# Optimization experiments

Hardware: AMD Instinct MI355X
Metric: run time of the kernel (lower is better)

## Reference

```python
import jax, jax.numpy as jnp
import numpy as np

# Static multi-scale pyramid (H, W) per level
SPATIAL_SHAPES = [(100, 100), (50, 50), (25, 25), (13, 13), (7, 7)]
D, H, L, P = 256, 8, 5, 4   # d_model, heads, levels, points
HD = D // H
B = 4
LQ = sum(h * w for h, w in SPATIAL_SHAPES)  # 13343
DFF = 2048


def layer_norm(x, g, b, eps=1e-5):
    m = x.mean(-1, keepdims=True)
    v = ((x - m) ** 2).mean(-1, keepdims=True)
    return (x - m) / jnp.sqrt(v + eps) * g + b


def ms_deform_attn_core(value, loc, attn):
    """value: [B, Lin, H, HD]; loc: [B, LQ, H, L, P, 2] in [0,1]; attn: [B, LQ, H, L, P].
    Bilinear sampling matches F.grid_sample(align_corners=False, padding_mode='zeros')."""
    out = jnp.zeros((B, H, LQ, HD), dtype=value.dtype)
    start = 0
    for lvl, (H_, W_) in enumerate(SPATIAL_SHAPES):
        val = value[:, start:start + H_ * W_]            # [B, HW, H, HD]
        start += H_ * W_
        val = val.transpose(0, 2, 1, 3)                   # [B, H, HW, HD]
        l = loc[:, :, :, lvl]                             # [B, LQ, H, P, 2]
        px = l[..., 0] * W_ - 0.5                         # grid_sample unnormalize
        py = l[..., 1] * H_ - 0.5
        x0 = jnp.floor(px)
        y0 = jnp.floor(py)
        wx1 = px - x0
        wy1 = py - y0
        x0i = x0.astype(jnp.int32)
        y0i = y0.astype(jnp.int32)
        samples = jnp.zeros((B, H, LQ, P, HD), dtype=value.dtype)
        for dy in (0, 1):
            for dx in (0, 1):
                xi = x0i + dx
                yi = y0i + dy
                w = (wx1 if dx else 1.0 - wx1) * (wy1 if dy else 1.0 - wy1)
                valid = (xi >= 0) & (xi < W_) & (yi >= 0) & (yi < H_)
                idx = jnp.clip(yi, 0, H_ - 1) * W_ + jnp.clip(xi, 0, W_ - 1)  # [B, LQ, H, P]
                idx_t = idx.transpose(0, 2, 1, 3).reshape(B, H, LQ * P)
                g = jnp.take_along_axis(val, idx_t[..., None], axis=2)        # [B, H, LQ*P, HD]
                g = g.reshape(B, H, LQ, P, HD)
                w_t = jnp.where(valid, w, 0.0).transpose(0, 2, 1, 3)          # [B, H, LQ, P]
                samples = samples + g * w_t[..., None]
        aw = attn[:, :, :, lvl].transpose(0, 2, 1, 3)     # [B, H, LQ, P]
        out = out + jnp.sum(samples * aw[..., None], axis=3)
    return out.transpose(0, 2, 1, 3).reshape(B, LQ, H * HD)


def setup_inputs() -> dict:
    key = jax.random.key(0)
    ks = jax.random.split(key, 24)
    s = 0.02
    inp = {
        'src': jax.random.normal(ks[0], (B, LQ, D), jnp.float32),
        'pos': jax.random.normal(ks[1], (B, LQ, D), jnp.float32),
        'reference_points': jax.random.uniform(ks[2], (B, LQ, L, 2), jnp.float32),
        'spatial_shapes': jnp.array(SPATIAL_SHAPES, dtype=jnp.int32),
        'level_start_index': jnp.array(np.cumsum([0] + [h * w for h, w in SPATIAL_SHAPES[:-1]]), dtype=jnp.int32),
        'W_off': jax.random.normal(ks[3], (D, H * L * P * 2), jnp.float32) * s,
        'b_off': jax.random.normal(ks[4], (H * L * P * 2,), jnp.float32) * s,
        'W_attn': jax.random.normal(ks[5], (D, H * L * P), jnp.float32) * s,
        'b_attn': jax.random.normal(ks[6], (H * L * P,), jnp.float32) * s,
        'W_val': jax.random.normal(ks[7], (D, D), jnp.float32) * s,
        'b_val': jax.random.normal(ks[8], (D,), jnp.float32) * s,
        'W_out': jax.random.normal(ks[9], (D, D), jnp.float32) * s,
        'b_out': jax.random.normal(ks[10], (D,), jnp.float32) * s,
        'g1': jnp.ones((D,), jnp.float32),
        'beta1': jnp.zeros((D,), jnp.float32),
        'W1': jax.random.normal(ks[11], (D, DFF), jnp.float32) * s,
        'bl1': jax.random.normal(ks[12], (DFF,), jnp.float32) * s,
        'W2': jax.random.normal(ks[13], (DFF, D), jnp.float32) * s,
        'bl2': jax.random.normal(ks[14], (D,), jnp.float32) * s,
        'g2': jnp.ones((D,), jnp.float32),
        'beta2': jnp.zeros((D,), jnp.float32),
    }
    return inp


def reference(src, pos, reference_points, spatial_shapes, level_start_index,
              W_off, b_off, W_attn, b_attn, W_val, b_val, W_out, b_out,
              g1, beta1, W1, bl1, W2, bl2, g2, beta2):
    q = src + pos                                                    # with_pos_embed
    off = (q @ W_off + b_off).reshape(B, LQ, H, L, P, 2)
    attn = jax.nn.softmax((q @ W_attn + b_attn).reshape(B, LQ, H, L * P), axis=-1)
    attn = attn.reshape(B, LQ, H, L, P)
    value = (src @ W_val + b_val).reshape(B, LQ, H, HD)
    # offset normalizer is (W, H) per level
    norm = jnp.array([[w, h] for h, w in SPATIAL_SHAPES], dtype=src.dtype)  # [L, 2]
    loc = reference_points[:, :, None, :, None, :] + off / norm[None, None, None, :, None, :]
    attn_out = ms_deform_attn_core(value, loc, attn) @ W_out + b_out
    x = layer_norm(src + attn_out, g1, beta1)                        # dropout = identity (eval)
    ffn = jax.nn.relu(x @ W1 + bl1) @ W2 + bl2
    return layer_norm(x + ffn, g2, beta2)
```

## Files before the change

### kernel.cpp

```cpp
#include <hip/hip_runtime.h>
#include <hip/hip_bf16.h>

typedef __bf16 bf16_t;
typedef __bf16 bf16x8 __attribute__((ext_vector_type(8)));
typedef float f32x4 __attribute__((ext_vector_type(4)));

#define B_    4
#define LQ_   13343
#define D_    256
#define H_    8
#define HD_   32
#define DFF_  2048
#define M_    (B_ * LQ_)

__device__ __forceinline__ int xcd_swz(int orig, int nwg) {
  int q = nwg >> 3, r = nwg & 7;
  int xcd = orig & 7, idx = orig >> 3;
  return (xcd < r ? xcd * (q + 1) : r * (q + 1) + (xcd - r) * q) + idx;
}

#define BM 128
#define BN 128
#define BK 32

#define MODE_F32       0
#define MODE_BF16      2
#define MODE_BF16_RELU 3

__device__ __forceinline__ void gload_lds16(const void* g, void* l) {
  __builtin_amdgcn_global_load_lds(
      (const __attribute__((address_space(1))) void*)g,
      (__attribute__((address_space(3))) void*)l, 16, 0, 0);
}

template <int MODE, bool AF32>
__global__ __launch_bounds__(256) void gemm_bt(
    const void* __restrict__ Av, int lda,
    const bf16_t* __restrict__ Bt, int ldb,
    const float* __restrict__ bias,
    void* __restrict__ Cv, int ldc,
    int M, int N, int K)
{
  __shared__ alignas(16) bf16_t As[2][BM * BK];
  __shared__ alignas(16) bf16_t Bs[2][BN * BK];
  const int tid  = threadIdx.x;
  const int wave = tid >> 6, lane = tid & 63;
  const int nyb = (N + BN - 1) / BN;
  const int gid = xcd_swz(blockIdx.x, (int)gridDim.x);
  const int m0 = (gid / nyb) * BM;
  const int n0 = (gid - (gid / nyb) * nyb) * BN;
  const int wm = (wave & 1) * 64;
  const int wn = (wave >> 1) * 64;
  const int lrow = lane & 15;
  const int quad = lane >> 4;

  const int srow = wave * 16 + (lane >> 2);
  const int scol = (lane & 3) * 8;
  const bf16_t* Ab = (const bf16_t*)Av;
  const float*  Af = (const float*)Av;

  const int ar0 = min(m0 + srow,      M - 1);
  const int ar1 = min(m0 + srow + 64, M - 1);
  const int br0 = min(n0 + srow,      N - 1);
  const int br1 = min(n0 + srow + 64, N - 1);

  const int r0 = tid >> 2;
  const int kc = (tid & 3) * 8;
  const int arw0 = min(m0 + r0,      M - 1);
  const int arw1 = min(m0 + r0 + 64, M - 1);

  auto stage_async = [&](int ke, int buf) {
    if (!AF32) {
      gload_lds16(Ab + (size_t)ar0 * lda + ke + scol, &As[buf][wave * 512]);
      gload_lds16(Ab + (size_t)ar1 * lda + ke + scol, &As[buf][2048 + wave * 512]);
    }
    gload_lds16(Bt + (size_t)br0 * ldb + ke + scol, &Bs[buf][wave * 512]);
    gload_lds16(Bt + (size_t)br1 * ldb + ke + scol, &Bs[buf][2048 + wave * 512]);
  };

  if (AF32) {
    const f32x4* p0 = (const f32x4*)(Af + (size_t)arw0 * lda + kc);
    const f32x4* p1 = (const f32x4*)(Af + (size_t)arw1 * lda + kc);
    f32x4 u0 = p0[0], w0 = p0[1], u1 = p1[0], w1 = p1[1];
    bf16x8 a0, a1;
#pragma unroll
    for (int j = 0; j < 4; ++j) {
      a0[j] = (bf16_t)u0[j]; a0[j + 4] = (bf16_t)w0[j];
      a1[j] = (bf16_t)u1[j]; a1[j + 4] = (bf16_t)w1[j];
    }
    *(bf16x8*)(&As[0][r0 * BK + kc])        = a0;
    *(bf16x8*)(&As[0][(r0 + 64) * BK + kc]) = a1;
  }
  stage_async(0, 0);
  __syncthreads();

  f32x4 acc[4][4] = {};
  const int nkt = K / BK;
  for (int kt = 0; kt < nkt; ++kt) {
    const int cur = kt & 1, nxt = cur ^ 1;
    const bool more = (kt + 1) < nkt;
    f32x4 u0 = {}, w0 = {}, u1 = {}, w1 = {};
    if (more) {
      const int ke = (kt + 1) * BK;
      if (AF32) {
        const f32x4* p0 = (const f32x4*)(Af + (size_t)arw0 * lda + ke + kc);
        const f32x4* p1 = (const f32x4*)(Af + (size_t)arw1 * lda + ke + kc);
        u0 = p0[0]; w0 = p0[1]; u1 = p1[0]; w1 = p1[1];
      }
      stage_async(ke, nxt);
    }
    bf16x8 af[4], bfr[4];
#pragma unroll
    for (int i = 0; i < 4; ++i)
      af[i] = *(const bf16x8*)(&As[cur][(wm + i * 16 + lrow) * BK + quad * 8]);
#pragma unroll
    for (int j = 0; j < 4; ++j)
      bfr[j] = *(const bf16x8*)(&Bs[cur][(wn + j * 16 + lrow) * BK + quad * 8]);
#pragma unroll
    for (int i = 0; i < 4; ++i)
#pragma unroll
      for (int j = 0; j < 4; ++j)
        acc[i][j] = __builtin_amdgcn_mfma_f32_16x16x32_bf16(af[i], bfr[j], acc[i][j], 0, 0, 0);
    if (more && AF32) {
      bf16x8 a0, a1;
#pragma unroll
      for (int j = 0; j < 4; ++j) {
        a0[j] = (bf16_t)u0[j]; a0[j + 4] = (bf16_t)w0[j];
        a1[j] = (bf16_t)u1[j]; a1[j + 4] = (bf16_t)w1[j];
      }
      *(bf16x8*)(&As[nxt][r0 * BK + kc])        = a0;
      *(bf16x8*)(&As[nxt][(r0 + 64) * BK + kc]) = a1;
    }
    __syncthreads();
  }

  float*  Cf = (float*)Cv;
  bf16_t* Cb = (bf16_t*)Cv;
#pragma unroll
  for (int i = 0; i < 4; ++i) {
#pragma unroll
    for (int j = 0; j < 4; ++j) {
      int gn = n0 + wn + j * 16 + lrow;
      if (gn >= N) continue;
      float bv = bias ? bias[gn] : 0.f;
#pragma unroll
      for (int r = 0; r < 4; ++r) {
        int gm = m0 + wm + i * 16 + quad * 4 + r;
        if (gm >= M) continue;
        float v = acc[i][j][r] + bv;
        size_t ci = (size_t)gm * ldc + gn;
        if (MODE == MODE_F32)       Cf[ci] = v;
        else if (MODE == MODE_BF16) Cb[ci] = (bf16_t)v;
        else                        Cb[ci] = (bf16_t)(v > 0.f ? v : 0.f);
      }
    }
  }
}

__global__ __launch_bounds__(256) void gemm_qkv(
    const float* __restrict__ src, const float* __restrict__ pos,
    const bf16_t* __restrict__ Bt,
    const float* __restrict__ b_off, const float* __restrict__ b_attn,
    bf16_t* __restrict__ offb, float* __restrict__ attnb)
{
  __shared__ alignas(16) bf16_t As[2][BM * BK];
  __shared__ alignas(16) bf16_t Bs[2][BN * BK];
  const int tid  = threadIdx.x;
  const int wave = tid >> 6, lane = tid & 63;
  const int gid = xcd_swz(blockIdx.x, (int)gridDim.x);
  const int m0 = (gid >> 2) * BM;
  const int n0 = (gid & 3) * BN;
  const int wm = (wave & 1) * 64;
  const int wn = (wave >> 1) * 64;
  const int lrow = lane & 15;
  const int quad = lane >> 4;
  const int N = 480;

  const int srow = wave * 16 + (lane >> 2);
  const int scol = (lane & 3) * 8;
  const int br0 = min(n0 + srow,      N - 1);
  const int br1 = min(n0 + srow + 64, N - 1);
  const int r0 = tid >> 2;
  const int kc = (tid & 3) * 8;
  const int arw0 = min(m0 + r0,      M_ - 1);
  const int arw1 = min(m0 + r0 + 64, M_ - 1);

  auto stageB = [&](int ke, int buf) {
    gload_lds16(Bt + (size_t)br0 * 256 + ke + scol, &Bs[buf][wave * 512]);
    gload_lds16(Bt + (size_t)br1 * 256 + ke + scol, &Bs[buf][2048 + wave * 512]);
  };
  auto loadA = [&](int ke, f32x4& u0, f32x4& w0, f32x4& u1, f32x4& w1) {
    const f32x4* s0 = (const f32x4*)(src + (size_t)arw0 * 256 + ke + kc);
    const f32x4* p0 = (const f32x4*)(pos + (size_t)arw0 * 256 + ke + kc);
    const f32x4* s1 = (const f32x4*)(src + (size_t)arw1 * 256 + ke + kc);
    const f32x4* p1 = (const f32x4*)(pos + (size_t)arw1 * 256 + ke + kc);
    u0 = s0[0] + p0[0]; w0 = s0[1] + p0[1];
    u1 = s1[0] + p1[0]; w1 = s1[1] + p1[1];
  };
  auto writeA = [&](int buf, f32x4 u0, f32x4 w0, f32x4 u1, f32x4 w1) {
    bf16x8 a0, a1;
#pragma unroll
    for (int j = 0; j < 4; ++j) {
      a0[j] = (bf16_t)u0[j]; a0[j + 4] = (bf16_t)w0[j];
      a1[j] = (bf16_t)u1[j]; a1[j + 4] = (bf16_t)w1[j];
    }
    *(bf16x8*)(&As[buf][r0 * BK + kc])        = a0;
    *(bf16x8*)(&As[buf][(r0 + 64) * BK + kc]) = a1;
  };

  { f32x4 u0, w0, u1, w1; loadA(0, u0, w0, u1, w1); writeA(0, u0, w0, u1, w1); }
  stageB(0, 0);
  __syncthreads();

  f32x4 acc[4][4] = {};
  for (int kt = 0; kt < 8; ++kt) {
    const int cur = kt & 1, nxt = cur ^ 1;
    const bool more = kt < 7;
    f32x4 u0 = {}, w0 = {}, u1 = {}, w1 = {};
    if (more) { loadA((kt + 1) * BK, u0, w0, u1, w1); stageB((kt + 1) * BK, nxt); }
    bf16x8 af[4], bfr[4];
#pragma unroll
    for (int i = 0; i < 4; ++i)
      af[i] = *(const bf16x8*)(&As[cur][(wm + i * 16 + lrow) * BK + quad * 8]);
#pragma unroll
    for (int j = 0; j < 4; ++j)
      bfr[j] = *(const bf16x8*)(&Bs[cur][(wn + j * 16 + lrow) * BK + quad * 8]);
#pragma unroll
    for (int i = 0; i < 4; ++i)
#pragma unroll
      for (int j = 0; j < 4; ++j)
        acc[i][j] = __builtin_amdgcn_mfma_f32_16x16x32_bf16(af[i], bfr[j], acc[i][j], 0, 0, 0);
    if (more) writeA(nxt, u0, w0, u1, w1);
    __syncthreads();
  }

#pragma unroll
  for (int i = 0; i < 4; ++i) {
#pragma unroll
    for (int j = 0; j < 4; ++j) {
      int gn = n0 + wn + j * 16 + lrow;
      if (gn >= N) continue;
      float bv = (gn < 320) ? b_off[gn] : b_attn[gn - 320];
#pragma unroll
      for (int r = 0; r < 4; ++r) {
        int gm = m0 + wm + i * 16 + quad * 4 + r;
        if (gm >= M_) continue;
        float v = acc[i][j][r] + bv;
        if (gn < 320) offb[(size_t)gm * 320 + gn] = (bf16_t)v;
        else          attnb[(size_t)gm * 160 + gn - 320] = v;
      }
    }
  }
}

__global__ __launch_bounds__(256) void k_ffn(
    const bf16_t* __restrict__ x,
    const bf16_t* __restrict__ w1t,
    const float* __restrict__ bl1,
    const bf16_t* __restrict__ w2t,
    float* __restrict__ outf)
{
  __shared__ alignas(16) bf16_t xs[8][64 * 32];
  __shared__ alignas(16) bf16_t hs[4][64 * 32];
  __shared__ alignas(16) bf16_t wst[2][256 * 32];
  const int tid  = threadIdx.x;
  const int wave = tid >> 6, lane = tid & 63;
  const int lrow = lane & 15, quad = lane >> 4;
  const int m0 = xcd_swz(blockIdx.x, (int)gridDim.x) * 64;
  const int srow = lane >> 2;
  const int scol = (lane & 3) * 8;
  const int wc0 = wave * 64;

  auto stage_w1 = [&](int hc, int kt, int buf) {
#pragma unroll
    for (int c = 0; c < 2; ++c) {
      int r = c * 64 + wave * 16 + srow;
      gload_lds16(w1t + (size_t)(hc * 128 + r) * 256 + kt * 32 + scol,
                  &wst[buf][c * 2048 + wave * 512]);
    }
  };
  auto stage_w2 = [&](int hc, int kt2, int buf) {
#pragma unroll
    for (int c = 0; c < 4; ++c) {
      int r = c * 64 + wave * 16 + srow;
      gload_lds16(w2t + (size_t)r * 2048 + hc * 128 + kt2 * 32 + scol,
                  &wst[buf][c * 2048 + wave * 512]);
    }
  };

  {
    int gr = min(m0 + wave * 16 + srow, M_ - 1);
#pragma unroll
    for (int c = 0; c < 8; ++c)
      gload_lds16(x + (size_t)gr * 256 + c * 32 + scol, &xs[c][wave * 512]);
  }
  stage_w1(0, 0, 0);
  __syncthreads();

  f32x4 cacc[4][4] = {};
  int s = 0;
  for (int hc = 0; hc < 16; ++hc) {
    float b0 = bl1[hc * 128 + wave * 32 + lrow];
    float b1 = bl1[hc * 128 + wave * 32 + 16 + lrow];
    f32x4 hacc[4][2] = {};
    for (int kt = 0; kt < 8; ++kt) {
      const int cur = s & 1, nxt = cur ^ 1;
      if (kt < 7) stage_w1(hc, kt + 1, nxt);
      else        stage_w2(hc, 0, nxt);
      bf16x8 af[4], bf[2];
#pragma unroll
      for (int i = 0; i < 4; ++i)
        af[i] = *(const bf16x8*)(&xs[kt][(i * 16 + lrow) * 32 + quad * 8]);
#pragma unroll
      for (int j = 0; j < 2; ++j)
        bf[j] = *(const bf16x8*)(&wst[cur][(wave * 32 + j * 16 + lrow) * 32 + quad * 8]);
#pragma unroll
      for (int i = 0; i < 4; ++i)
#pragma unroll
        for (int j = 0; j < 2; ++j)
          hacc[i][j] = __builtin_amdgcn_mfma_f32_16x16x32_bf16(af[i], bf[j], hacc[i][j], 0, 0, 0);
      if (kt == 7) {
#pragma unroll
        for (int i = 0; i < 4; ++i)
#pragma unroll
          for (int j = 0; j < 2; ++j) {
            float bb = j ? b1 : b0;
#pragma unroll
            for (int r = 0; r < 4; ++r) {
              float v = hacc[i][j][r] + bb;
              hs[wave][(i * 16 + quad * 4 + r) * 32 + j * 16 + lrow] =
                  (bf16_t)(v > 0.f ? v : 0.f);
            }
          }
      }
      __syncthreads();
      ++s;
    }
    for (int kt2 = 0; kt2 < 4; ++kt2) {
      const int cur = s & 1, nxt = cur ^ 1;
      if (kt2 < 3)      stage_w2(hc, kt2 + 1, nxt);
      else if (hc < 15) stage_w1(hc + 1, 0, nxt);
      bf16x8 af2[4], bf2[4];
#pragma unroll
      for (int i = 0; i < 4; ++i)
        af2[i] = *(const bf16x8*)(&hs[kt2][(i * 16 + lrow) * 32 + quad * 8]);
#pragma unroll
      for (int j = 0; j < 4; ++j)
        bf2[j] = *(const bf16x8*)(&wst[cur][(wc0 + j * 16 + lrow) * 32 + quad * 8]);
#pragma unroll
      for (int i = 0; i < 4; ++i)
#pragma unroll
        for (int j = 0; j < 4; ++j)
          cacc[i][j] = __builtin_amdgcn_mfma_f32_16x16x32_bf16(af2[i], bf2[j], cacc[i][j], 0, 0, 0);
      __syncthreads();
      ++s;
    }
  }

#pragma unroll
  for (int i = 0; i < 4; ++i)
#pragma unroll
    for (int j = 0; j < 4; ++j)
#pragma unroll
      for (int r = 0; r < 4; ++r) {
        int gm = m0 + i * 16 + quad * 4 + r;
        if (gm < M_) outf[(size_t)gm * 256 + wc0 + j * 16 + lrow] = cacc[i][j][r];
      }
}

__global__ __launch_bounds__(256) void k_transpose_all(
    const float* __restrict__ i0, const float* __restrict__ i1,
    const float* __restrict__ i2, const float* __restrict__ i3,
    const float* __restrict__ i4, const float* __restrict__ i5,
    bf16_t* __restrict__ o0, bf16_t* __restrict__ o1, bf16_t* __restrict__ o2,
    bf16_t* __restrict__ o3, bf16_t* __restrict__ o4, bf16_t* __restrict__ o5)
{
  int bid = blockIdx.x;
  const float* in; bf16_t* out; int K, N, txn;
  if (bid < 80)        { in = i0; out = o0; K = 256;  N = 320;  txn = 10; }
  else if (bid < 120)  { in = i1; out = o1; K = 256;  N = 160;  bid -= 80;  txn = 5; }
  else if (bid < 184)  { in = i2; out = o2; K = 256;  N = 256;  bid -= 120; txn = 8; }
  else if (bid < 248)  { in = i3; out = o3; K = 256;  N = 256;  bid -= 184; txn = 8; }
  else if (bid < 760)  { in = i4; out = o4; K = 256;  N = 2048; bid -= 248; txn = 64; }
  else                 { in = i5; out = o5; K = 2048; N = 256;  bid -= 760; txn = 8; }
  const int bx = bid % txn, by = bid / txn;
  __shared__ float tile[32][33];
  const int k0 = by * 32, n0 = bx * 32;
  const int tx = threadIdx.x & 31, ty = threadIdx.x >> 5;
#pragma unroll
  for (int r = ty; r < 32; r += 8)
    tile[r][tx] = in[(size_t)(k0 + r) * N + n0 + tx];
  __syncthreads();
#pragma unroll
  for (int r = ty; r < 32; r += 8)
    out[(size_t)(n0 + r) * K + k0 + tx] = (bf16_t)tile[tx][r];
}

__global__ __launch_bounds__(256) void k_sample(
    const bf16_t* __restrict__ value,
    const bf16_t* __restrict__ off,
    const float* __restrict__ attn,
    const float* __restrict__ rp,
    bf16_t* __restrict__ core)
{
  const int Wl[5] = {100, 50, 25, 13, 7};
  const int st[5] = {0, 10000, 12500, 13125, 13294};
  __shared__ alignas(16) bf16_t s_off[8][320];
  __shared__ alignas(16) float  s_attn[8][160];
  __shared__ float s_rp[8][10];
  const int t = threadIdx.x;
  const int bq0 = xcd_swz(blockIdx.x, (int)gridDim.x) * 8;
  for (int i = t; i < 320; i += 256) {
    int q = i / 40, e = i - q * 40;
    if (bq0 + q < M_) {
      *(bf16x8*)&s_off[q][e * 8] = *(const bf16x8*)(off + (size_t)(bq0 + q) * 320 + e * 8);
      *(f32x4*)&s_attn[q][e * 4] = *(const f32x4*)(attn + (size_t)(bq0 + q) * 160 + e * 4);
    }
  }
  if (t < 80) {
    int q = t / 10, e = t - q * 10;
    if (bq0 + q < M_) s_rp[q][e] = rp[(size_t)(bq0 + q) * 10 + e];
  }
  __syncthreads();
  if (t < 64) {
    float* p = &s_attn[t >> 3][(t & 7) * 20];
    float mx = p[0];
#pragma unroll
    for (int i = 1; i < 20; ++i) mx = fmaxf(mx, p[i]);
    float e[20], sum = 0.f;
#pragma unroll
    for (int i = 0; i < 20; ++i) { e[i] = expf(p[i] - mx); sum += e[i]; }
    float inv = 1.f / sum;
#pragma unroll
    for (int i = 0; i < 20; ++i) p[i] = e[i] * inv;
  }
  __syncthreads();

  const int wq = t >> 5, s = t & 31;
  const int h = s >> 2, d0 = (s & 3) * 8;
  const int bq = bq0 + wq;
  if (bq >= M_) return;
  const int b = bq / LQ_;
  const bf16_t* vbase = value + ((size_t)b * LQ_) * 256 + h * 32 + d0;
  float acc[8] = {};
#pragma unroll
  for (int lvl = 0; lvl < 5; ++lvl) {
    const float W = (float)Wl[lvl];
    const float rx = s_rp[wq][lvl * 2], ry = s_rp[wq][lvl * 2 + 1];
#pragma unroll
    for (int p = 0; p < 4; ++p) {
      const int base = (h * 5 + lvl) * 4 + p;
      float px = rx * W + (float)s_off[wq][base * 2]     - 0.5f;
      float py = ry * W + (float)s_off[wq][base * 2 + 1] - 0.5f;
      float aw = s_attn[wq][h * 20 + lvl * 4 + p];
      float x0f = floorf(px), y0f = floorf(py);
      float wx1 = px - x0f, wy1 = py - y0f;
      int x0 = (int)x0f, y0 = (int)y0f;
#pragma unroll
      for (int dy = 0; dy < 2; ++dy) {
        int yi = y0 + dy;
        bool vy = (yi >= 0) & (yi < Wl[lvl]);
        int yc = min(max(yi, 0), Wl[lvl] - 1);
        float wy = dy ? wy1 : 1.f - wy1;
#pragma unroll
        for (int dx = 0; dx < 2; ++dx) {
          int xi = x0 + dx;
          bool vx = (xi >= 0) & (xi < Wl[lvl]);
          int xc = min(max(xi, 0), Wl[lvl] - 1);
          float cw = (vx & vy) ? aw * wy * (dx ? wx1 : 1.f - wx1) : 0.f;
          bf16x8 v = *(const bf16x8*)(vbase + (size_t)(st[lvl] + yc * Wl[lvl] + xc) * 256);
#pragma unroll
          for (int j = 0; j < 8; ++j) acc[j] += cw * (float)v[j];
        }
      }
    }
  }
  bf16x8 o;
#pragma unroll
  for (int j = 0; j < 8; ++j) o[j] = (bf16_t)acc[j];
  *(bf16x8*)(core + (size_t)bq * 256 + h * 32 + d0) = o;
}

template <typename TA, typename TR, typename TO>
__global__ __launch_bounds__(256) void k_ln4(
    const TA* __restrict__ a, const TR* __restrict__ res,
    const float* __restrict__ eb, const float* __restrict__ g,
    const float* __restrict__ beta, TO* __restrict__ out, int rows)
{
  const int wave = threadIdx.x >> 6, lane = threadIdx.x & 63;
  const int row = blockIdx.x * 4 + wave;
  if (row >= rows) return;
  const size_t base = (size_t)row * 256 + lane * 4;
  float v[4];
#pragma unroll
  for (int j = 0; j < 4; ++j) {
    v[j] = (float)a[base + j] + (float)res[base + j];
    if (eb) v[j] += eb[lane * 4 + j];
  }
  float s1 = v[0] + v[1] + v[2] + v[3];
  float s2 = v[0] * v[0] + v[1] * v[1] + v[2] * v[2] + v[3] * v[3];
#pragma unroll
  for (int o = 32; o > 0; o >>= 1) { s1 += __shfl_xor(s1, o); s2 += __shfl_xor(s2, o); }
  float m = s1 * (1.f / 256.f);
  float var = s2 * (1.f / 256.f) - m * m;
  float inv = rsqrtf(var + 1e-5f);
#pragma unroll
  for (int j = 0; j < 4; ++j)
    out[base + j] = (TO)(((v[j] - m) * inv) * g[lane * 4 + j] + beta[lane * 4 + j]);
}

extern "C" void kernel_launch(void* const* d_in, const int* in_sizes, int n_in,
                              void* d_out, int out_size, void* d_ws, size_t ws_size,
                              hipStream_t stream) {
  const float* src   = (const float*)d_in[0];
  const float* pos   = (const float*)d_in[1];
  const float* rp    = (const float*)d_in[2];
  const float* W_off = (const float*)d_in[5];
  const float* b_off = (const float*)d_in[6];
  const float* W_attn= (const float*)d_in[7];
  const float* b_attn= (const float*)d_in[8];
  const float* W_val = (const float*)d_in[9];
  const float* b_val = (const float*)d_in[10];
  const float* W_out = (const float*)d_in[11];
  const float* b_out = (const float*)d_in[12];
  const float* g1    = (const float*)d_in[13];
  const float* beta1 = (const float*)d_in[14];
  const float* W1    = (const float*)d_in[15];
  const float* bl1   = (const float*)d_in[16];
  const float* W2    = (const float*)d_in[17];
  const float* bl2   = (const float*)d_in[18];
  const float* g2    = (const float*)d_in[19];
  const float* beta2 = (const float*)d_in[20];

  char* ws = (char*)d_ws;
  const size_t SZ_TOK = (size_t)M_ * 256 * 2;
  const size_t SZ_ATT = (size_t)M_ * 160 * 4;

  size_t o = 0;
  bf16_t* wTqkv = (bf16_t*)(ws + o); o += 480 * 256 * 2;
  bf16_t* wTval = (bf16_t*)(ws + o); o += 256 * 256 * 2;
  bf16_t* wTout = (bf16_t*)(ws + o); o += 256 * 256 * 2;
  bf16_t* wT1   = (bf16_t*)(ws + o); o += 2048 * 256 * 2;
  bf16_t* wT2   = (bf16_t*)(ws + o); o += 2048 * 256 * 2;
  o = (o + 255) & ~(size_t)255;
  char* Areg = ws + o; o += SZ_TOK;
  char* Creg = ws + o; o += SZ_ATT;
  char* Dreg = ws + o; o += SZ_TOK;

  bf16_t* coreb   = (bf16_t*)Areg;
  float*  attnb   = (float*) Creg;
  bf16_t* attn_out= (bf16_t*)Creg;
  bf16_t* valb    = (bf16_t*)Dreg;
  bf16_t* xbuf    = (bf16_t*)Dreg;
  bf16_t* offb    = (bf16_t*)d_out;
  float*  outf    = (float*) d_out;

  k_transpose_all<<<dim3(1272), 256, 0, stream>>>(
      W_off, W_attn, W_val, W_out, W1, W2,
      wTqkv, wTqkv + 320 * 256, wTval, wTout, wT1, wT2);

  dim3 blk(256);
  const int gM = (M_ + BM - 1) / BM;

  gemm_qkv<<<dim3(gM * 4), blk, 0, stream>>>(src, pos, wTqkv, b_off, b_attn, offb, attnb);
  gemm_bt<MODE_BF16, true><<<dim3(gM * 2), blk, 0, stream>>>(src, 256, wTval, 256, b_val, valb, 256, M_, 256, 256);
  k_sample<<<dim3((M_ + 7) / 8), blk, 0, stream>>>(valb, offb, attnb, rp, coreb);
  gemm_bt<MODE_BF16, false><<<dim3(gM * 2), blk, 0, stream>>>(coreb, 256, wTout, 256, b_out, attn_out, 256, M_, 256, 256);
  k_ln4<float, bf16_t, bf16_t><<<dim3((M_ + 3) / 4), blk, 0, stream>>>(src, attn_out, (const float*)nullptr, g1, beta1, xbuf, M_);

  k_ffn<<<dim3((M_ + 63) / 64), blk, 0, stream>>>(xbuf, wT1, bl1, wT2, outf);

  k_ln4<bf16_t, float, float><<<dim3((M_ + 3) / 4), blk, 0, stream>>>(xbuf, outf, bl2, g2, beta2, outf, M_);
}
```

Baseline: 711.4 us.

## Load FFN weights directly from global to registers and swizzle LDS tiles

Removes the double-buffered LDS weight staging in the fused FFN kernel. Each wave now reads its W1/W2 fragments straight from global memory (relying on L2 since all blocks share the weights), and the per-k-step barriers are dropped. The x and hidden tiles in LDS use an XOR swizzle to avoid bank conflicts, and the launch bounds ask for 3 blocks per CU now that LDS use is smaller. The risk is higher global and L2 load latency on the MFMA critical path with no prefetching, and possible register pressure from the occupancy hint.

Result: slower. 786.2 us (+10.5%).

```diff
diff --git a/kernel.cpp b/kernel.cpp
--- a/kernel.cpp
+++ b/kernel.cpp
@@ -253,7 +253,8 @@
   }
 }
 
-__global__ __launch_bounds__(256) void k_ffn(
+#define SWZ(row, byte) ((byte) ^ (((row) & 7) << 4))
+__global__ __launch_bounds__(256, 3) void k_ffn(
     const bf16_t* __restrict__ x,
     const bf16_t* __restrict__ w1t,
     const float* __restrict__ bl1,
@@ -262,7 +263,6 @@
 {
   __shared__ alignas(16) bf16_t xs[8][64 * 32];
   __shared__ alignas(16) bf16_t hs[4][64 * 32];
-  __shared__ alignas(16) bf16_t wst[2][256 * 32];
   const int tid  = threadIdx.x;
   const int wave = tid >> 6, lane = tid & 63;
   const int lrow = lane & 15, quad = lane >> 4;
@@ -271,89 +271,82 @@
   const int scol = (lane & 3) * 8;
   const int wc0 = wave * 64;
 
-  auto stage_w1 = [&](int hc, int kt, int buf) {
-#pragma unroll
-    for (int c = 0; c < 2; ++c) {
-      int r = c * 64 + wave * 16 + srow;
-      gload_lds16(w1t + (size_t)(hc * 128 + r) * 256 + kt * 32 + scol,
-                  &wst[buf][c * 2048 + wave * 512]);
-    }
-  };
-  auto stage_w2 = [&](int hc, int kt2, int buf) {
-#pragma unroll
-    for (int c = 0; c < 4; ++c) {
-      int r = c * 64 + wave * 16 + srow;
-      gload_lds16(w2t + (size_t)r * 2048 + hc * 128 + kt2 * 32 + scol,
-                  &wst[buf][c * 2048 + wave * 512]);
-    }
-  };
-
   {
-    int gr = min(m0 + wave * 16 + srow, M_ - 1);
-#pragma unroll
-    for (int c = 0; c < 8; ++c)
-      gload_lds16(x + (size_t)gr * 256 + c * 32 + scol, &xs[c][wave * 512]);
-  }
-  stage_w1(0, 0, 0);
+    const int row = wave * 16 + srow;
+    const int gr = min(m0 + row, M_ - 1);
+    const int wb = SWZ(row, row * 64 + scol * 2);
+#pragma unroll
+    for (int c = 0; c < 8; ++c) {
+      bf16x8 v = *(const bf16x8*)(x + (size_t)gr * 256 + c * 32 + scol);
+      *(bf16x8*)((char*)&xs[c][0] + wb) = v;
+    }
+  }
+
+  const bf16_t* w1r0 = w1t + (size_t)(wave * 32 + lrow) * 256 + quad * 8;
+  const bf16_t* w1r1 = w1t + (size_t)(wave * 32 + 16 + lrow) * 256 + quad * 8;
+  const bf16_t* w2r0 = w2t + (size_t)(wc0 + lrow) * 2048 + quad * 8;
+  const bf16_t* w2r1 = w2r0 + (size_t)16 * 2048;
+  const bf16_t* w2r2 = w2r0 + (size_t)32 * 2048;
+  const bf16_t* w2r3 = w2r0 + (size_t)48 * 2048;
+
   __syncthreads();
 
   f32x4 cacc[4][4] = {};
-  int s = 0;
   for (int hc = 0; hc < 16; ++hc) {
-    float b0 = bl1[hc * 128 + wave * 32 + lrow];
-    float b1 = bl1[hc * 128 + wave * 32 + 16 + lrow];
+    const float b0 = bl1[hc * 128 + wave * 32 + lrow];
+    const float b1 = bl1[hc * 128 + wave * 32 + 16 + lrow];
+    const size_t w1off = (size_t)hc * 128 * 256;
     f32x4 hacc[4][2] = {};
+#pragma unroll
     for (int kt = 0; kt < 8; ++kt) {
-      const int cur = s & 1, nxt = cur ^ 1;
-      if (kt < 7) stage_w1(hc, kt + 1, nxt);
-      else        stage_w2(hc, 0, nxt);
-      bf16x8 af[4], bf[2];
-#pragma unroll
-      for (int i = 0; i < 4; ++i)
-        af[i] = *(const bf16x8*)(&xs[kt][(i * 16 + lrow) * 32 + quad * 8]);
-#pragma unroll
-      for (int j = 0; j < 2; ++j)
-        bf[j] = *(const bf16x8*)(&wst[cur][(wave * 32 + j * 16 + lrow) * 32 + quad * 8]);
-#pragma unroll
-      for (int i = 0; i < 4; ++i)
-#pragma unroll
-        for (int j = 0; j < 2; ++j)
-          hacc[i][j] = __builtin_amdgcn_mfma_f32_16x16x32_bf16(af[i], bf[j], hacc[i][j], 0, 0, 0);
-      if (kt == 7) {
-#pragma unroll
-        for (int i = 0; i < 4; ++i)
-#pragma unroll
-          for (int j = 0; j < 2; ++j) {
-            float bb = j ? b1 : b0;
-#pragma unroll
-            for (int r = 0; r < 4; ++r) {
-              float v = hacc[i][j][r] + bb;
-              hs[wave][(i * 16 + quad * 4 + r) * 32 + j * 16 + lrow] =
-                  (bf16_t)(v > 0.f ? v : 0.f);
-            }
-          }
-      }
-      __syncthreads();
-      ++s;
-    }
+      bf16x8 bf0 = *(const bf16x8*)(w1r0 + w1off + kt * 32);
+      bf16x8 bf1 = *(const bf16x8*)(w1r1 + w1off + kt * 32);
+      bf16x8 af[4];
+#pragma unroll
+      for (int i = 0; i < 4; ++i) {
+        const int row = i * 16 + lrow;
+        af[i] = *(const bf16x8*)((char*)&xs[kt][0] + SWZ(row, row * 64 + quad * 16));
+      }
+#pragma unroll
+      for (int i = 0; i < 4; ++i) {
+        hacc[i][0] = __builtin_amdgcn_mfma_f32_16x16x32_bf16(af[i], bf0, hacc[i][0], 0, 0, 0);
+        hacc[i][1] = __builtin_amdgcn_mfma_f32_16x16x32_bf16(af[i], bf1, hacc[i][1], 0, 0, 0);
+      }
+    }
+    __syncthreads();
+#pragma unroll
+    for (int i = 0; i < 4; ++i)
+#pragma unroll
+      for (int j = 0; j < 2; ++j) {
+        const float bb = j ? b1 : b0;
+#pragma unroll
+        for (int r = 0; r < 4; ++r) {
+          float v = hacc[i][j][r] + bb;
+          const int row = i * 16 + quad * 4 + r;
+          *(bf16_t*)((char*)&hs[wave][0] + SWZ(row, row * 64 + (j * 16 + lrow) * 2)) =
+              (bf16_t)(v > 0.f ? v : 0.f);
+        }
+      }
+    __syncthreads();
+    const size_t w2off = (size_t)hc * 128;
+#pragma unroll
     for (int kt2 = 0; kt2 < 4; ++kt2) {
-      const int cur = s & 1, nxt = cur ^ 1;
-      if (kt2 < 3)      stage_w2(hc, kt2 + 1, nxt);
-      else if (hc < 15) stage_w1(hc + 1, 0, nxt);
-      bf16x8 af2[4], bf2[4];
-#pragma unroll
-      for (int i = 0; i < 4; ++i)
-        af2[i] = *(const bf16x8*)(&hs[kt2][(i * 16 + lrow) * 32 + quad * 8]);
-#pragma unroll
-      for (int j = 0; j < 4; ++j)
-        bf2[j] = *(const bf16x8*)(&wst[cur][(wc0 + j * 16 + lrow) * 32 + quad * 8]);
+      bf16x8 bf2[4];
+      bf2[0] = *(const bf16x8*)(w2r0 + w2off + kt2 * 32);
+      bf2[1] = *(const bf16x8*)(w2r1 + w2off + kt2 * 32);
+      bf2[2] = *(const bf16x8*)(w2r2 + w2off + kt2 * 32);
+      bf2[3] = *(const bf16x8*)(w2r3 + w2off + kt2 * 32);
+      bf16x8 af2[4];
+#pragma unroll
+      for (int i = 0; i < 4; ++i) {
+        const int row = i * 16 + lrow;
+        af2[i] = *(const bf16x8*)((char*)&hs[kt2][0] + SWZ(row, row * 64 + quad * 16));
+      }
 #pragma unroll
       for (int i = 0; i < 4; ++i)
 #pragma unroll
         for (int j = 0; j < 4; ++j)
           cacc[i][j] = __builtin_amdgcn_mfma_f32_16x16x32_bf16(af2[i], bf2[j], cacc[i][j], 0, 0, 0);
-      __syncthreads();
-      ++s;
     }
   }
 
```
